# Performance work log

Measured on AMD Instinct MI355X. Metric: run time of the kernel, lower is better.

Reference implementation:

```python
import jax, jax.numpy as jnp
import numpy as np

B, N, D = 4, 2048, 1024
H, HD = 16, 64
S = 11  # n_scales
D4 = jnp.array([0.4829629131445341, 0.8365163037378079,
                0.2241438680420134, -0.1294095225512604], dtype=jnp.float32)


def _causal_dilated_d4(f, d):
    """Causal depthwise D4 conv with dilation d along axis 2. f: [B,H,N,HD].
    Matches torch F.pad(x,(3d,0)) + F.conv1d(dilation=d, groups=C):
    y[n] = sum_t D4[t] * f[n - (3-t)*d]."""
    n = f.shape[2]
    fp = jnp.pad(f, ((0, 0), (0, 0), (3 * d, 0), (0, 0)))
    return (D4[0] * fp[:, :, 0:n, :]
            + D4[1] * fp[:, :, d:d + n, :]
            + D4[2] * fp[:, :, 2 * d:2 * d + n, :]
            + D4[3] * fp[:, :, 3 * d:3 * d + n, :])


def setup_inputs() -> dict:
    key = jax.random.key(0)
    ks = jax.random.split(key, 10)
    s = 0.02
    return {
        "x": jax.random.normal(ks[0], (B, N, D), dtype=jnp.float32),
        "Wqkv": jax.random.normal(ks[1], (3 * D, D), dtype=jnp.float32) * s,
        "bqkv": jnp.zeros((3 * D,), dtype=jnp.float32),
        "Wo": jax.random.normal(ks[2], (D, D), dtype=jnp.float32) * s,
        "bo": jnp.zeros((D,), dtype=jnp.float32),
        "Wg": jax.random.normal(ks[3], (D, D), dtype=jnp.float32) * s,
        "bg": jnp.full((D,), 2.0, dtype=jnp.float32),
        "scale_gain": jnp.zeros((S, H), dtype=jnp.float32),
        "Wqs": jax.random.normal(ks[4], (S, HD), dtype=jnp.float32) * 0.01,
        "field_coupling": jnp.eye(H, dtype=jnp.float32)
        + 0.01 * jax.random.normal(ks[5], (H, H), dtype=jnp.float32),
    }


def reference(x, Wqkv, bqkv, Wo, bo, Wg, bg, scale_gain, Wqs, field_coupling):
    b, n, d = x.shape
    qkv = x @ Wqkv.T + bqkv                          # [B,N,3D]
    q, k, v = jnp.split(qkv, 3, axis=-1)
    q = q.reshape(b, n, H, HD).transpose(0, 2, 1, 3)  # [B,H,N,HD]
    k = k.reshape(b, n, H, HD).transpose(0, 2, 1, 3)
    v = v.reshape(b, n, H, HD).transpose(0, 2, 1, 3)

    # per-position scale gains: learned prior + query-conditioned offset
    q_offset = jnp.einsum('bhnd,sd->bhns', q, Wqs)    # [B,H,N,S]
    prior = scale_gain.T[None, :, None, :]            # [1,H,1,S]
    gains = jax.nn.softmax(q_offset + prior, axis=-1)

    # deposit: field[i] = V[i] * ||K[i]||
    k_mag = jnp.linalg.norm(k, axis=-1, keepdims=True)
    field = v * k_mag                                 # [B,H,N,HD]

    # propagate: causal multiscale dilated D4 conv, gain-weighted accumulate
    out_field = jnp.zeros_like(field)
    for j in range(S):
        y = _causal_dilated_d4(field, 1 << j)
        out_field = out_field + gains[:, :, :, j:j + 1] * y

    coupling = jax.nn.softmax(field_coupling, axis=-1)
    out_field = jnp.einsum('ij,bjnd->bind', coupling, out_field)

    gate = jax.nn.sigmoid(x @ Wg.T + bg)              # [B,N,D]
    gathered = out_field.transpose(0, 2, 1, 3).reshape(b, n, d)
    return (gathered * gate) @ Wo.T + bo
```

## Files before the change

### kernel.cpp

```cpp
#include <hip/hip_runtime.h>
#include <hip/hip_bf16.h>
#include <stdint.h>
#include <math.h>

#define BB 4
#define NN 2048
#define DD 1024
#define HH 16
#define HDD 64
#define SS 11

#define D4_0 0.4829629131445341f
#define D4_1 0.8365163037378079f
#define D4_2 0.2241438680420134f
#define D4_3 (-0.1294095225512604f)

typedef __bf16 bf16_t;
typedef __bf16 bf16x4_t __attribute__((ext_vector_type(4)));
typedef __bf16 bf16x8_t __attribute__((ext_vector_type(8)));
typedef float f32x4_t __attribute__((ext_vector_type(4)));

__global__ __launch_bounds__(256) void cvt_all_k(const float* __restrict__ s0,
                                                 const float* __restrict__ s1,
                                                 const float* __restrict__ s2,
                                                 const float* __restrict__ s3,
                                                 bf16_t* __restrict__ d0,
                                                 bf16_t* __restrict__ d1,
                                                 bf16_t* __restrict__ d2,
                                                 bf16_t* __restrict__ d3) {
  const int n0 = 2097152, n1 = 786432, n2 = 262144, n3 = 262144;
  int i = blockIdx.x * 256 + threadIdx.x;
  const float* s;
  bf16_t* d;
  if (i < n0) { s = s0; d = d0; }
  else if (i < n0 + n1) { i -= n0; s = s1; d = d1; }
  else if (i < n0 + n1 + n2) { i -= n0 + n1; s = s2; d = d2; }
  else { i -= n0 + n1 + n2; if (i >= n3) return; s = s3; d = d3; }
  f32x4_t v = ((const f32x4_t*)s)[i];
  bf16x4_t o;
  o[0] = (bf16_t)v[0]; o[1] = (bf16_t)v[1]; o[2] = (bf16_t)v[2]; o[3] = (bf16_t)v[3];
  ((bf16x4_t*)d)[i] = o;
}

__device__ __forceinline__ void gload16(const void* g, void* l) {
  __builtin_amdgcn_global_load_lds((__attribute__((address_space(1))) void*)(void*)g,
                                   (__attribute__((address_space(3))) void*)l,
                                   16, 0, 0);
}

__global__ __launch_bounds__(512, 2) void gemm256(const bf16_t* __restrict__ Aa,
                                                  const bf16_t* __restrict__ Bw,
                                                  const float* __restrict__ bias0,
                                                  const float* __restrict__ bias1,
                                                  bf16_t* __restrict__ out0,
                                                  bf16_t* __restrict__ out1) {
  __shared__ bf16_t sA[2][16384];
  __shared__ bf16_t sB[2][16384];

  const int tid = threadIdx.x;
  const int s = (blockIdx.x & 7) * 64 + (blockIdx.x >> 3);
  const int mtile = s >> 4;
  const int ntile = s & 15;
  const int row0 = mtile << 8;
  const int col0 = ntile << 8;

  const int w = tid >> 6, lane = tid & 63;
  const int wm = w >> 2, wn = w & 3;
  const int wmbase = wm << 7;
  const int wnbase = wn << 6;
  const int m16 = lane & 15, quad = lane >> 4;

  f32x4_t acc[8][4];
#pragma unroll
  for (int i = 0; i < 8; i++)
#pragma unroll
    for (int jq = 0; jq < 4; jq++) acc[i][jq] = (f32x4_t){0.f, 0.f, 0.f, 0.f};

  auto stage_half = [&](int buf, int tensor, int half, int t) {
    if (t >= 16) return;
    const bf16_t* gb = tensor ? Bw : Aa;
    const int gr0 = (tensor ? col0 : row0) + (half << 7);
    const int kb = t << 6;
    bf16_t* lbase = (tensor ? sB[buf] : sA[buf]) + (half << 13);
#pragma unroll
    for (int l = 0; l < 2; ++l) {
      int c = l * 512 + tid;
      int row = c >> 3, kc = c & 7;
      int swz = kc ^ (row & 7);
      const bf16_t* g = gb + (size_t)(gr0 + row) * 1024 + kb + swz * 8;
      bf16_t* lp = lbase + ((l * 512 + (tid & 448)) << 3);
      gload16(g, lp);
    }
  };

  bf16x8_t bA[2][4], bB[2][4];
  auto rdA = [&](int bank, int buf, int ih, int ks) {
#pragma unroll
    for (int i = 0; i < 4; i++) {
      int ar = wmbase + ((ih * 4 + i) << 4) + m16;
      int kc = (ks << 2) + quad;
      bA[bank][i] = *(const bf16x8_t*)&sA[buf][ar * 64 + ((kc ^ (ar & 7)) << 3)];
    }
  };
  auto rdB = [&](int bank, int buf, int ks) {
#pragma unroll
    for (int jq = 0; jq < 4; jq++) {
      int br = wnbase + (jq << 4) + m16;
      int kc = (ks << 2) + quad;
      bB[bank][jq] = *(const bf16x8_t*)&sB[buf][br * 64 + ((kc ^ (br & 7)) << 3)];
    }
  };
  auto domfma = [&](int ab, int bb, int ih) {
#pragma unroll
    for (int i = 0; i < 4; i++)
#pragma unroll
      for (int jq = 0; jq < 4; jq++)
        acc[ih * 4 + i][jq] =
            __builtin_amdgcn_mfma_f32_16x16x32_bf16(bA[ab][i], bB[bb][jq], acc[ih * 4 + i][jq], 0, 0, 0);
  };

#define BAR() __builtin_amdgcn_s_barrier()
#define WAITL4() asm volatile("s_waitcnt lgkmcnt(4)" ::: "memory"); __builtin_amdgcn_sched_barrier(0)
#define WAITL8() asm volatile("s_waitcnt lgkmcnt(8)" ::: "memory"); __builtin_amdgcn_sched_barrier(0)
#define WAITL0() asm volatile("s_waitcnt lgkmcnt(0)" ::: "memory"); __builtin_amdgcn_sched_barrier(0)
#define PRIO1() __builtin_amdgcn_s_setprio(1)
#define PRIO0() __builtin_amdgcn_s_setprio(0)
#define WAITV0() asm volatile("s_waitcnt vmcnt(0)" ::: "memory")

  stage_half(0, 0, 0, 0); stage_half(0, 0, 1, 0);
  stage_half(0, 1, 0, 0); stage_half(0, 1, 1, 0);
  stage_half(1, 1, 0, 1); stage_half(1, 1, 1, 1);
  asm volatile("s_waitcnt vmcnt(4)" ::: "memory");
  BAR();
  rdA(0, 0, 0, 0); rdB(0, 0, 0);
  WAITL0();

  for (int it = 0; it < 8; ++it) {
    const int Tb = 2 * it + 1, T2 = 2 * it + 2, T3 = 2 * it + 3;
    const bool lastit = (it == 7);
    rdA(1, 0, 1, 0);
    stage_half(1, 0, 0, Tb); stage_half(1, 0, 1, Tb);
    BAR(); WAITL4(); PRIO1(); domfma(0, 0, 0); PRIO0(); BAR();
    rdA(0, 0, 0, 1); rdB(1, 0, 1);
    BAR(); WAITL8(); PRIO1(); domfma(1, 0, 1); PRIO0(); BAR();
    rdA(1, 0, 1, 1);
    BAR(); WAITL4(); PRIO1(); domfma(0, 1, 0); PRIO0(); WAITV0(); BAR();
    rdA(0, 1, 0, 0); rdB(0, 1, 0);
    stage_half(0, 1, 0, T2); stage_half(0, 1, 1, T2);
    BAR(); WAITL8(); PRIO1(); domfma(1, 1, 1); PRIO0(); BAR();
    rdA(1, 1, 1, 0);
    stage_half(0, 0, 0, T2); stage_half(0, 0, 1, T2);
    BAR(); WAITL4(); PRIO1(); domfma(0, 0, 0); PRIO0(); BAR();
    rdA(0, 1, 0, 1); rdB(1, 1, 1);
    BAR(); WAITL8(); PRIO1(); domfma(1, 0, 1); PRIO0(); BAR();
    rdA(1, 1, 1, 1);
    BAR(); WAITL4(); PRIO1(); domfma(0, 1, 0); PRIO0(); WAITV0(); BAR();
    if (!lastit) { rdA(0, 0, 0, 0); rdB(0, 0, 0); }
    stage_half(1, 1, 0, T3); stage_half(1, 1, 1, T3);
    BAR();
    if (!lastit) { WAITL8(); } else { WAITL0(); }
    PRIO1(); domfma(1, 1, 1); PRIO0(); BAR();
  }
#undef BAR
#undef WAITL4
#undef WAITL8
#undef WAITL0
#undef PRIO1
#undef PRIO0
#undef WAITV0

  const bool is_gate = (col0 >= 3072);
#pragma unroll
  for (int i = 0; i < 8; i++) {
#pragma unroll
    for (int jq = 0; jq < 4; jq++) {
      const int grow0 = row0 + wmbase + (i << 4) + (quad << 2);
      const int gcol = col0 + wnbase + (jq << 4) + m16;
      const float bval = is_gate ? bias1[gcol - 3072] : bias0[gcol];
#pragma unroll
      for (int r = 0; r < 4; r++) {
        float val = acc[i][jq][r] + bval;
        if (is_gate)
          out1[(size_t)(grow0 + r) * 1024 + (gcol - 3072)] =
              (bf16_t)(1.f / (1.f + __expf(-val)));
        else
          out0[(size_t)(grow0 + r) * 3072 + gcol] = (bf16_t)val;
      }
    }
  }
}

template <int MODE>
__global__ __launch_bounds__(256) void gemm_nt(const bf16_t* __restrict__ A,
                                               const bf16_t* __restrict__ Bw,
                                               const float* __restrict__ bias0,
                                               const float* __restrict__ bias1,
                                               void* __restrict__ out0v,
                                               void* __restrict__ out1v,
                                               int M, int Nn, int K) {
  __shared__ bf16_t As[128 * 64];
  __shared__ bf16_t Bs[128 * 64];

  const int tid = threadIdx.x;
  const int ntiles = Nn >> 7;
  const int grp = ntiles << 3;
  const int g = blockIdx.x / grp;
  const int j = blockIdx.x % grp;
  const int mtile = (g << 3) | (j & 7);
  const int ntile = j >> 3;
  const int row0 = mtile << 7;
  const int col0 = ntile << 7;
  const int w = tid >> 6, lane = tid & 63;
  const int wm = w >> 1, wn = w & 1;
  const int m16 = lane & 15, quad = lane >> 4;

  f32x4_t acc[4][4];
#pragma unroll
  for (int i = 0; i < 4; i++)
#pragma unroll
    for (int jj = 0; jj < 4; jj++) acc[i][jj] = (f32x4_t){0.f, 0.f, 0.f, 0.f};

  for (int kb = 0; kb < K; kb += 64) {
    __syncthreads();
#pragma unroll
    for (int r = 0; r < 4; ++r) {
      int c = r * 256 + tid;
      int row = c >> 3, kc = c & 7;
      int swz = kc ^ (row & 7);
      const bf16_t* gpA = A + (size_t)(row0 + row) * K + kb + swz * 8;
      const bf16_t* gpB = Bw + (size_t)(col0 + row) * K + kb + swz * 8;
      bf16_t* lpA = As + (size_t)(r * 256 + (tid & 192)) * 8;
      bf16_t* lpB = Bs + (size_t)(r * 256 + (tid & 192)) * 8;
      gload16(gpA, lpA);
      gload16(gpB, lpB);
    }
    __syncthreads();

#pragma unroll
    for (int kk = 0; kk < 2; ++kk) {
      bf16x8_t af[4], bfr[4];
      const int kc = (kk << 2) + quad;
#pragma unroll
      for (int i = 0; i < 4; i++) {
        int arow = (wm << 6) + (i << 4) + m16;
        af[i] = *(const bf16x8_t*)(As + arow * 64 + ((kc ^ (arow & 7)) << 3));
        int brow = (wn << 6) + (i << 4) + m16;
        bfr[i] = *(const bf16x8_t*)(Bs + brow * 64 + ((kc ^ (brow & 7)) << 3));
      }
#pragma unroll
      for (int i = 0; i < 4; i++)
#pragma unroll
        for (int jj = 0; jj < 4; jj++)
          acc[i][jj] = __builtin_amdgcn_mfma_f32_16x16x32_bf16(af[i], bfr[jj], acc[i][jj], 0, 0, 0);
    }
  }

#pragma unroll
  for (int i = 0; i < 4; i++) {
#pragma unroll
    for (int jj = 0; jj < 4; jj++) {
      const int grow0 = row0 + (wm << 6) + (i << 4) + (quad << 2);
      const int gcol = col0 + (wn << 6) + (jj << 4) + m16;
      const float bval = (MODE == 0)
                             ? (gcol < 3072 ? bias0[gcol] : bias1[gcol - 3072])
                             : bias0[gcol];
#pragma unroll
      for (int r = 0; r < 4; r++) {
        float val = acc[i][jj][r] + bval;
        if (MODE == 0) {
          if (gcol < 3072)
            ((bf16_t*)out0v)[(size_t)(grow0 + r) * 3072 + gcol] = (bf16_t)val;
          else
            ((bf16_t*)out1v)[(size_t)(grow0 + r) * 1024 + (gcol - 3072)] =
                (bf16_t)(1.f / (1.f + __expf(-val)));
        } else {
          ((float*)out0v)[(size_t)(grow0 + r) * Nn + gcol] = val;
        }
      }
    }
  }
}

__global__ __launch_bounds__(256) void field_gains_k(const bf16_t* __restrict__ qkvb,
                                                     const float* __restrict__ scale_gain,
                                                     const float* __restrict__ Wqs,
                                                     bf16_t* __restrict__ fieldb,
                                                     float* __restrict__ gains) {
  __shared__ float skmag[4 * 16];
  const int tid = threadIdx.x;
  const int w = tid >> 6, lane = tid & 63;
  const int bn = blockIdx.x * 4 + w;
  const int b = bn >> 11, n_pos = bn & 2047;
  const int m16 = lane & 15, quad = lane >> 4;
  const bf16_t* qp = qkvb + (size_t)bn * 3072;

  bf16x8_t aq[2], ak[2], bw[2];
#pragma unroll
  for (int it = 0; it < 2; it++) {
    const int koff = it * 32 + quad * 8;
    aq[it] = *(const bf16x8_t*)(qp + m16 * 64 + koff);
    ak[it] = *(const bf16x8_t*)(qp + 1024 + m16 * 64 + koff);
    bf16x8_t bwv;
    if (m16 < SS) {
      const float* wp = Wqs + m16 * 64 + koff;
#pragma unroll
      for (int j = 0; j < 8; j++) bwv[j] = (bf16_t)wp[j];
    } else {
#pragma unroll
      for (int j = 0; j < 8; j++) bwv[j] = (bf16_t)0.f;
    }
    bw[it] = bwv;
  }

  f32x4_t acc_l = (f32x4_t){0.f, 0.f, 0.f, 0.f};
  f32x4_t acc_k = (f32x4_t){0.f, 0.f, 0.f, 0.f};
#pragma unroll
  for (int it = 0; it < 2; it++) {
    acc_l = __builtin_amdgcn_mfma_f32_16x16x32_bf16(aq[it], bw[it], acc_l, 0, 0, 0);
    acc_k = __builtin_amdgcn_mfma_f32_16x16x32_bf16(ak[it], ak[it], acc_k, 0, 0, 0);
  }

#pragma unroll
  for (int r = 0; r < 4; r++) {
    if (m16 == quad * 4 + r) skmag[w * 16 + m16] = sqrtf(fmaxf(acc_k[r], 0.f));
  }

#pragma unroll
  for (int r = 0; r < 4; r++) {
    const int m = quad * 4 + r;
    float lg = (m16 < SS) ? (acc_l[r] + scale_gain[m16 * 16 + m]) : -1e30f;
    float mx = lg;
#pragma unroll
    for (int sh = 1; sh < 16; sh <<= 1) mx = fmaxf(mx, __shfl_xor(mx, sh, 64));
    float e = (m16 < SS) ? __expf(lg - mx) : 0.f;
    float se = e;
#pragma unroll
    for (int sh = 1; sh < 16; sh <<= 1) se += __shfl_xor(se, sh, 64);
    if (m16 < SS)
      gains[((size_t)(b * 16 + m) * 2048 + n_pos) * SS + m16] = e / se;
  }

  __syncthreads();

#pragma unroll
  for (int h = 0; h < 16; h++) {
    const float km = skmag[w * 16 + h];
    const float v = (float)qp[2048 + h * 64 + lane];
    fieldb[((size_t)(b * 16 + h) * 2048 + n_pos) * 64 + lane] = (bf16_t)(v * km);
  }
}

__global__ __launch_bounds__(256) void conv_k(const bf16_t* __restrict__ field,
                                              const float* __restrict__ gains,
                                              bf16_t* __restrict__ facc) {
  __shared__ float sg[32 * SS];
  const int tid = threadIdx.x;
  const int blk = blockIdx.x;
  const int bh = blk & 63;
  const int ntile = blk >> 6;
  const int n0 = ntile * 32;

  for (int i = tid; i < 32 * SS; i += 256)
    sg[i] = gains[((size_t)bh * 2048 + n0) * SS + i];
  __syncthreads();

  const int w = tid >> 6, lane = tid & 63;
  const int nsub = lane >> 3, c = lane & 7;
  const int ln = w * 8 + nsub;
  const int n = n0 + ln;
  const bf16_t* frow = field + (size_t)bh * 2048 * 64;

  float g[SS];
#pragma unroll
  for (int s = 0; s < SS; s++) g[s] = sg[ln * SS + s];

  float acc[8];
  {
    bf16x8_t f0 = *(const bf16x8_t*)(frow + (size_t)n * 64 + c * 8);
#pragma unroll
    for (int q = 0; q < 8; q++) acc[q] = D4_3 * (float)f0[q];
  }
#pragma unroll
  for (int j = 0; j < 11; j++) {
    float wgt = D4_2 * g[j];
    if (j >= 1) wgt += D4_1 * g[j - 1];
    int rr = n - (1 << j);
    float wv = rr >= 0 ? wgt : 0.f;
    rr = rr >= 0 ? rr : 0;
    bf16x8_t fv = *(const bf16x8_t*)(frow + (size_t)rr * 64 + c * 8);
#pragma unroll
    for (int q = 0; q < 8; q++) acc[q] += wv * (float)fv[q];
  }
#pragma unroll
  for (int j = 0; j < 10; j++) {
    int rr = n - (3 << j);
    float wv = rr >= 0 ? (D4_0 * g[j]) : 0.f;
    rr = rr >= 0 ? rr : 0;
    bf16x8_t fv = *(const bf16x8_t*)(frow + (size_t)rr * 64 + c * 8);
#pragma unroll
    for (int q = 0; q < 8; q++) acc[q] += wv * (float)fv[q];
  }
  bf16x8_t o;
#pragma unroll
  for (int q = 0; q < 8; q++) o[q] = (bf16_t)acc[q];
  *(bf16x8_t*)(facc + ((size_t)bh * 2048 + n) * 64 + c * 8) = o;
}

__global__ __launch_bounds__(1024) void couple_gate_k(const bf16_t* __restrict__ facc,
                                                      const float* __restrict__ fcoup,
                                                      const bf16_t* __restrict__ gate,
                                                      bf16_t* __restrict__ gmat) {
  __shared__ float sacc[1024];
  __shared__ float sc[256];
  __shared__ float scn[256];
  const int tid = threadIdx.x;
  const int bn = blockIdx.x;
  const int b = bn >> 11, n = bn & 2047;
  if (tid < 256) sc[tid] = fcoup[tid];
  const int i = tid >> 6, hd = tid & 63;
  sacc[tid] = (float)facc[(((size_t)(b * 16 + i)) * 2048 + n) * 64 + hd];
  __syncthreads();
  if (tid < 16) {
    float row[16];
    float mx = -1e30f;
#pragma unroll
    for (int j = 0; j < 16; j++) { row[j] = sc[tid * 16 + j]; mx = fmaxf(mx, row[j]); }
    float se = 0.f;
#pragma unroll
    for (int j = 0; j < 16; j++) { row[j] = __expf(row[j] - mx); se += row[j]; }
    float inv = 1.f / se;
#pragma unroll
    for (int j = 0; j < 16; j++) scn[tid * 16 + j] = row[j] * inv;
  }
  __syncthreads();
  float s = 0.f;
#pragma unroll
  for (int j = 0; j < 16; j++) s += scn[i * 16 + j] * sacc[j * 64 + hd];
  const float gt = (float)gate[(size_t)bn * 1024 + tid];
  gmat[(size_t)bn * 1024 + tid] = (bf16_t)(s * gt);
}

extern "C" void kernel_launch(void* const* d_in, const int* in_sizes, int n_in,
                              void* d_out, int out_size, void* d_ws, size_t ws_size,
                              hipStream_t stream) {
  (void)in_sizes; (void)n_in; (void)out_size; (void)ws_size;
  const float* x = (const float*)d_in[0];
  const float* Wqkv = (const float*)d_in[1];
  const float* bqkv = (const float*)d_in[2];
  const float* Wo = (const float*)d_in[3];
  const float* bo = (const float*)d_in[4];
  const float* Wg = (const float*)d_in[5];
  const float* bg = (const float*)d_in[6];
  const float* scale_gain = (const float*)d_in[7];
  const float* Wqs = (const float*)d_in[8];
  const float* fcoup = (const float*)d_in[9];

  char* ws = (char*)d_ws;
  size_t off = 0;
  auto alloc = [&](size_t bytes) {
    void* p = ws + off;
    off += (bytes + 255) & ~(size_t)255;
    return p;
  };
  bf16_t* xb = (bf16_t*)alloc(8192ull * 1024 * 2);
  bf16_t* Wab = (bf16_t*)alloc(4096ull * 1024 * 2);
  bf16_t* Wob = (bf16_t*)alloc(1024ull * 1024 * 2);
  bf16_t* qkvb = (bf16_t*)alloc(8192ull * 3072 * 2);
  bf16_t* gateb = (bf16_t*)alloc(8192ull * 1024 * 2);
  bf16_t* fieldb = (bf16_t*)alloc(8388608ull * 2);
  float* gains = (float*)alloc(8192ull * 16 * SS * 4);
  bf16_t* facc = (bf16_t*)alloc(8388608ull * 2);
  bf16_t* gmat = (bf16_t*)alloc(8192ull * 1024 * 2);

  cvt_all_k<<<13316, 256, 0, stream>>>(x, Wqkv, Wg, Wo,
                                       xb, Wab, Wab + 3072ull * 1024, Wob);

  gemm256<<<512, 512, 0, stream>>>(xb, Wab, bqkv, bg, qkvb, gateb);

  field_gains_k<<<2048, 256, 0, stream>>>(qkvb, scale_gain, Wqs, fieldb, gains);

  conv_k<<<4096, 256, 0, stream>>>(fieldb, gains, facc);

  couple_gate_k<<<8192, 1024, 0, stream>>>(facc, fcoup, gateb, gmat);

  gemm_nt<1><<<64 * 8, 256, 0, stream>>>(gmat, Wob, bo, nullptr, (void*)d_out, nullptr, 8192, 1024, 1024);
}
```

Before: 285.3 us.

## Fuse conv and head-coupling kernels; simplify GEMM main-loop pipeline

```diff
diff --git a/kernel.cpp b/kernel.cpp
--- a/kernel.cpp
+++ b/kernel.cpp
@@ -93,35 +93,33 @@
     }
   };
 
-  bf16x8_t bA[2][4], bB[2][4];
-  auto rdA = [&](int bank, int buf, int ih, int ks) {
-#pragma unroll
-    for (int i = 0; i < 4; i++) {
-      int ar = wmbase + ((ih * 4 + i) << 4) + m16;
+  bf16x8_t af[8], bfr[4];
+  auto rdA8 = [&](int buf, int ks) {
+#pragma unroll
+    for (int i = 0; i < 8; i++) {
+      int ar = wmbase + (i << 4) + m16;
       int kc = (ks << 2) + quad;
-      bA[bank][i] = *(const bf16x8_t*)&sA[buf][ar * 64 + ((kc ^ (ar & 7)) << 3)];
+      af[i] = *(const bf16x8_t*)&sA[buf][ar * 64 + ((kc ^ (ar & 7)) << 3)];
     }
   };
-  auto rdB = [&](int bank, int buf, int ks) {
+  auto rdB = [&](int buf, int ks) {
 #pragma unroll
     for (int jq = 0; jq < 4; jq++) {
       int br = wnbase + (jq << 4) + m16;
       int kc = (ks << 2) + quad;
-      bB[bank][jq] = *(const bf16x8_t*)&sB[buf][br * 64 + ((kc ^ (br & 7)) << 3)];
+      bfr[jq] = *(const bf16x8_t*)&sB[buf][br * 64 + ((kc ^ (br & 7)) << 3)];
     }
   };
-  auto domfma = [&](int ab, int bb, int ih) {
-#pragma unroll
-    for (int i = 0; i < 4; i++)
+  auto domfma32 = [&]() {
+#pragma unroll
+    for (int i = 0; i < 8; i++)
 #pragma unroll
       for (int jq = 0; jq < 4; jq++)
-        acc[ih * 4 + i][jq] =
-            __builtin_amdgcn_mfma_f32_16x16x32_bf16(bA[ab][i], bB[bb][jq], acc[ih * 4 + i][jq], 0, 0, 0);
+        acc[i][jq] =
+            __builtin_amdgcn_mfma_f32_16x16x32_bf16(af[i], bfr[jq], acc[i][jq], 0, 0, 0);
   };
 
 #define BAR() __builtin_amdgcn_s_barrier()
-#define WAITL4() asm volatile("s_waitcnt lgkmcnt(4)" ::: "memory"); __builtin_amdgcn_sched_barrier(0)
-#define WAITL8() asm volatile("s_waitcnt lgkmcnt(8)" ::: "memory"); __builtin_amdgcn_sched_barrier(0)
 #define WAITL0() asm volatile("s_waitcnt lgkmcnt(0)" ::: "memory"); __builtin_amdgcn_sched_barrier(0)
 #define PRIO1() __builtin_amdgcn_s_setprio(1)
 #define PRIO0() __builtin_amdgcn_s_setprio(0)
@@ -129,41 +127,25 @@
 
   stage_half(0, 0, 0, 0); stage_half(0, 0, 1, 0);
   stage_half(0, 1, 0, 0); stage_half(0, 1, 1, 0);
-  stage_half(1, 1, 0, 1); stage_half(1, 1, 1, 1);
-  asm volatile("s_waitcnt vmcnt(4)" ::: "memory");
+  WAITV0();
   BAR();
-  rdA(0, 0, 0, 0); rdB(0, 0, 0);
-  WAITL0();
 
   for (int it = 0; it < 8; ++it) {
-    const int Tb = 2 * it + 1, T2 = 2 * it + 2, T3 = 2 * it + 3;
-    const bool lastit = (it == 7);
-    rdA(1, 0, 1, 0);
-    stage_half(1, 0, 0, Tb); stage_half(1, 0, 1, Tb);
-    BAR(); WAITL4(); PRIO1(); domfma(0, 0, 0); PRIO0(); BAR();
-    rdA(0, 0, 0, 1); rdB(1, 0, 1);
-    BAR(); WAITL8(); PRIO1(); domfma(1, 0, 1); PRIO0(); BAR();
-    rdA(1, 0, 1, 1);
-    BAR(); WAITL4(); PRIO1(); domfma(0, 1, 0); PRIO0(); WAITV0(); BAR();
-    rdA(0, 1, 0, 0); rdB(0, 1, 0);
-    stage_half(0, 1, 0, T2); stage_half(0, 1, 1, T2);
-    BAR(); WAITL8(); PRIO1(); domfma(1, 1, 1); PRIO0(); BAR();
-    rdA(1, 1, 1, 0);
-    stage_half(0, 0, 0, T2); stage_half(0, 0, 1, T2);
-    BAR(); WAITL4(); PRIO1(); domfma(0, 0, 0); PRIO0(); BAR();
-    rdA(0, 1, 0, 1); rdB(1, 1, 1);
-    BAR(); WAITL8(); PRIO1(); domfma(1, 0, 1); PRIO0(); BAR();
-    rdA(1, 1, 1, 1);
-    BAR(); WAITL4(); PRIO1(); domfma(0, 1, 0); PRIO0(); WAITV0(); BAR();
-    if (!lastit) { rdA(0, 0, 0, 0); rdB(0, 0, 0); }
-    stage_half(1, 1, 0, T3); stage_half(1, 1, 1, T3);
-    BAR();
-    if (!lastit) { WAITL8(); } else { WAITL0(); }
-    PRIO1(); domfma(1, 1, 1); PRIO0(); BAR();
+    const int O = 2 * it + 1, E2 = 2 * it + 2;
+    rdA8(0, 0); rdB(0, 0);
+    stage_half(1, 0, 0, O); stage_half(1, 0, 1, O);
+    stage_half(1, 1, 0, O); stage_half(1, 1, 1, O);
+    BAR(); WAITL0(); PRIO1(); domfma32(); PRIO0(); BAR();
+    rdA8(0, 1); rdB(0, 1);
+    BAR(); WAITL0(); PRIO1(); domfma32(); PRIO0(); WAITV0(); BAR();
+    rdA8(1, 0); rdB(1, 0);
+    stage_half(0, 0, 0, E2); stage_half(0, 0, 1, E2);
+    stage_half(0, 1, 0, E2); stage_half(0, 1, 1, E2);
+    BAR(); WAITL0(); PRIO1(); domfma32(); PRIO0(); BAR();
+    rdA8(1, 1); rdB(1, 1);
+    BAR(); WAITL0(); PRIO1(); domfma32(); PRIO0(); WAITV0(); BAR();
   }
 #undef BAR
-#undef WAITL4
-#undef WAITL8
 #undef WAITL0
 #undef PRIO1
 #undef PRIO0
@@ -350,81 +332,24 @@
   }
 }
 
-__global__ __launch_bounds__(256) void conv_k(const bf16_t* __restrict__ field,
-                                              const float* __restrict__ gains,
-                                              bf16_t* __restrict__ facc) {
-  __shared__ float sg[32 * SS];
-  const int tid = threadIdx.x;
-  const int blk = blockIdx.x;
-  const int bh = blk & 63;
-  const int ntile = blk >> 6;
-  const int n0 = ntile * 32;
-
-  for (int i = tid; i < 32 * SS; i += 256)
-    sg[i] = gains[((size_t)bh * 2048 + n0) * SS + i];
-  __syncthreads();
-
-  const int w = tid >> 6, lane = tid & 63;
-  const int nsub = lane >> 3, c = lane & 7;
-  const int ln = w * 8 + nsub;
-  const int n = n0 + ln;
-  const bf16_t* frow = field + (size_t)bh * 2048 * 64;
-
-  float g[SS];
-#pragma unroll
-  for (int s = 0; s < SS; s++) g[s] = sg[ln * SS + s];
-
-  float acc[8];
-  {
-    bf16x8_t f0 = *(const bf16x8_t*)(frow + (size_t)n * 64 + c * 8);
-#pragma unroll
-    for (int q = 0; q < 8; q++) acc[q] = D4_3 * (float)f0[q];
-  }
-#pragma unroll
-  for (int j = 0; j < 11; j++) {
-    float wgt = D4_2 * g[j];
-    if (j >= 1) wgt += D4_1 * g[j - 1];
-    int rr = n - (1 << j);
-    float wv = rr >= 0 ? wgt : 0.f;
-    rr = rr >= 0 ? rr : 0;
-    bf16x8_t fv = *(const bf16x8_t*)(frow + (size_t)rr * 64 + c * 8);
-#pragma unroll
-    for (int q = 0; q < 8; q++) acc[q] += wv * (float)fv[q];
-  }
-#pragma unroll
-  for (int j = 0; j < 10; j++) {
-    int rr = n - (3 << j);
-    float wv = rr >= 0 ? (D4_0 * g[j]) : 0.f;
-    rr = rr >= 0 ? rr : 0;
-    bf16x8_t fv = *(const bf16x8_t*)(frow + (size_t)rr * 64 + c * 8);
-#pragma unroll
-    for (int q = 0; q < 8; q++) acc[q] += wv * (float)fv[q];
-  }
-  bf16x8_t o;
-#pragma unroll
-  for (int q = 0; q < 8; q++) o[q] = (bf16_t)acc[q];
-  *(bf16x8_t*)(facc + ((size_t)bh * 2048 + n) * 64 + c * 8) = o;
-}
-
-__global__ __launch_bounds__(1024) void couple_gate_k(const bf16_t* __restrict__ facc,
+__global__ __launch_bounds__(1024) void conv_couple_k(const bf16_t* __restrict__ field,
+                                                      const float* __restrict__ gains,
                                                       const float* __restrict__ fcoup,
                                                       const bf16_t* __restrict__ gate,
                                                       bf16_t* __restrict__ gmat) {
-  __shared__ float sacc[1024];
-  __shared__ float sc[256];
+  __shared__ bf16_t fld[16 * 16 * 64];
   __shared__ float scn[256];
   const int tid = threadIdx.x;
-  const int bn = blockIdx.x;
-  const int b = bn >> 11, n = bn & 2047;
-  if (tid < 256) sc[tid] = fcoup[tid];
-  const int i = tid >> 6, hd = tid & 63;
-  sacc[tid] = (float)facc[(((size_t)(b * 16 + i)) * 2048 + n) * 64 + hd];
-  __syncthreads();
+  const int blk = blockIdx.x;
+  const int b = blk >> 7;
+  const int nt = blk & 127;
+  const int n0 = nt * 16;
+
   if (tid < 16) {
     float row[16];
     float mx = -1e30f;
 #pragma unroll
-    for (int j = 0; j < 16; j++) { row[j] = sc[tid * 16 + j]; mx = fmaxf(mx, row[j]); }
+    for (int j = 0; j < 16; j++) { row[j] = fcoup[tid * 16 + j]; mx = fmaxf(mx, row[j]); }
     float se = 0.f;
 #pragma unroll
     for (int j = 0; j < 16; j++) { row[j] = __expf(row[j] - mx); se += row[j]; }
@@ -432,12 +357,75 @@
 #pragma unroll
     for (int j = 0; j < 16; j++) scn[tid * 16 + j] = row[j] * inv;
   }
+
+  const int w = tid >> 6, lane = tid & 63;
+  const int nsub = lane >> 3, c = lane & 7;
+  const bf16_t* frow = field + ((size_t)(b * 16 + w)) * 2048 * 64;
+
+#pragma unroll
+  for (int p = 0; p < 2; ++p) {
+    const int nl = p * 8 + nsub;
+    const int n = n0 + nl;
+    float g[SS];
+    const float* gp = gains + ((size_t)(b * 16 + w) * 2048 + n) * SS;
+#pragma unroll
+    for (int s = 0; s < SS; s++) g[s] = gp[s];
+
+    float acc[8];
+    {
+      bf16x8_t f0 = *(const bf16x8_t*)(frow + (size_t)n * 64 + c * 8);
+#pragma unroll
+      for (int q = 0; q < 8; q++) acc[q] = D4_3 * (float)f0[q];
+    }
+#pragma unroll
+    for (int j = 0; j < 11; j++) {
+      float wgt = D4_2 * g[j];
+      if (j >= 1) wgt += D4_1 * g[j - 1];
+      int rr = n - (1 << j);
+      float wv = rr >= 0 ? wgt : 0.f;
+      rr = rr >= 0 ? rr : 0;
+      bf16x8_t fv = *(const bf16x8_t*)(frow + (size_t)rr * 64 + c * 8);
+#pragma unroll
+      for (int q = 0; q < 8; q++) acc[q] += wv * (float)fv[q];
+    }
+#pragma unroll
+    for (int j = 0; j < 10; j++) {
+      int rr = n - (3 << j);
+      float wv = rr >= 0 ? (D4_0 * g[j]) : 0.f;
+      rr = rr >= 0 ? rr : 0;
+      bf16x8_t fv = *(const bf16x8_t*)(frow + (size_t)rr * 64 + c * 8);
+#pragma unroll
+      for (int q = 0; q < 8; q++) acc[q] += wv * (float)fv[q];
+    }
+    bf16x8_t o;
+#pragma unroll
+    for (int q = 0; q < 8; q++) o[q] = (bf16_t)acc[q];
+    *(bf16x8_t*)&fld[w * 1024 + nl * 64 + c * 8] = o;
+  }
+
   __syncthreads();
-  float s = 0.f;
-#pragma unroll
-  for (int j = 0; j < 16; j++) s += scn[i * 16 + j] * sacc[j * 64 + hd];
-  const float gt = (float)gate[(size_t)bn * 1024 + tid];
-  gmat[(size_t)bn * 1024 + tid] = (bf16_t)(s * gt);
+
+#pragma unroll
+  for (int p = 0; p < 2; ++p) {
+    const int nl = p * 8 + nsub;
+    const int n = n0 + nl;
+    float s8[8];
+#pragma unroll
+    for (int q = 0; q < 8; q++) s8[q] = 0.f;
+#pragma unroll
+    for (int j = 0; j < 16; j++) {
+      const float cw = scn[w * 16 + j];
+      bf16x8_t v = *(const bf16x8_t*)&fld[j * 1024 + nl * 64 + c * 8];
+#pragma unroll
+      for (int q = 0; q < 8; q++) s8[q] += cw * (float)v[q];
+    }
+    const size_t base = ((size_t)(b * 2048 + n)) * 1024 + w * 64 + c * 8;
+    bf16x8_t gt = *(const bf16x8_t*)(gate + base);
+    bf16x8_t o;
+#pragma unroll
+    for (int q = 0; q < 8; q++) o[q] = (bf16_t)(s8[q] * (float)gt[q]);
+    *(bf16x8_t*)(gmat + base) = o;
+  }
 }
 
 extern "C" void kernel_launch(void* const* d_in, const int* in_sizes, int n_in,
@@ -469,7 +457,6 @@
   bf16_t* gateb = (bf16_t*)alloc(8192ull * 1024 * 2);
   bf16_t* fieldb = (bf16_t*)alloc(8388608ull * 2);
   float* gains = (float*)alloc(8192ull * 16 * SS * 4);
-  bf16_t* facc = (bf16_t*)alloc(8388608ull * 2);
   bf16_t* gmat = (bf16_t*)alloc(8192ull * 1024 * 2);
 
   cvt_all_k<<<13316, 256, 0, stream>>>(x, Wqkv, Wg, Wo,
@@ -479,9 +466,7 @@
 
   field_gains_k<<<2048, 256, 0, stream>>>(qkvb, scale_gain, Wqs, fieldb, gains);
 
-  conv_k<<<4096, 256, 0, stream>>>(fieldb, gains, facc);
-
-  couple_gate_k<<<8192, 1024, 0, stream>>>(facc, fcoup, gateb, gmat);
+  conv_couple_k<<<512, 1024, 0, stream>>>(fieldb, gains, fcoup, gateb, gmat);
 
   gemm_nt<1><<<64 * 8, 256, 0, stream>>>(gmat, Wob, bo, nullptr, (void*)d_out, nullptr, 8192, 1024, 1024);
 }
```

Result: slower. 302.8 us (+6.1%).
